# Performance work log

Hardware: AMD Instinct MI355X
Metric: run time of the kernel (lower is better)

Reference implementation:

```python
import jax, jax.numpy as jnp
import numpy as np

# ---- config (mirrors init_kwargs) ----
H = 128
W = 128
FMO_STEPS = 4
INPUT_FRAMES = 1
N_PIECES = 1
N_TERMS = 2
CAM_DIST = 2.0
ROT_DIVIDE = 1.0
SIGMAINV = 7000.0
ERODE_K = 5
FOCAL = float(1.0 / np.tan(1.57 / 4.0))  # generate_perspective_projection(1.57/2), aspect=1


def quaternion_to_angle_axis(q):
    # q: [B,4] in (w,x,y,z) convention (torchgeometry)
    q1, q2, q3 = q[..., 1], q[..., 2], q[..., 3]
    sin_sq = q1 * q1 + q2 * q2 + q3 * q3
    sin_t = jnp.sqrt(sin_sq + 1e-20)
    cos_t = q[..., 0]
    two_theta = 2.0 * jnp.where(cos_t < 0.0, jnp.arctan2(-sin_t, -cos_t), jnp.arctan2(sin_t, cos_t))
    k = jnp.where(sin_sq > 1e-12, two_theta / sin_t, 2.0)
    return q[..., 1:4] * k[..., None]


def angle_axis_to_rotation_matrix(aa):
    # aa: [B,3] -> [B,3,3] (Rodrigues)
    th = jnp.sqrt(jnp.sum(aa * aa, axis=-1, keepdims=True) + 1e-12)  # [B,1]
    k = aa / th
    kx, ky, kz = k[..., 0], k[..., 1], k[..., 2]
    zero = jnp.zeros_like(kx)
    K = jnp.stack([jnp.stack([zero, -kz, ky], -1),
                   jnp.stack([kz, zero, -kx], -1),
                   jnp.stack([-ky, kx, zero], -1)], -2)
    s = jnp.sin(th)[..., None]
    c = jnp.cos(th)[..., None]
    return jnp.eye(3, dtype=aa.dtype) + s * K + (1.0 - c) * jnp.matmul(K, K)


def rasterize(fv_img, fv_z, face_feat, fn_z):
    # fv_img [B,F,3,2] NDC, fv_z [B,F,3] camera z, face_feat [B,F,3,C], fn_z [B,F]
    B, F = fv_img.shape[:2]
    xs = jnp.linspace(-1.0, 1.0, W)
    ys = jnp.linspace(1.0, -1.0, H)
    py, px = jnp.meshgrid(ys, xs, indexing='ij')  # [H,W]
    a, b, c = fv_img[:, :, 0], fv_img[:, :, 1], fv_img[:, :, 2]  # [B,F,2]
    e0 = b - a
    e1 = c - a
    denom = e0[..., 0] * e1[..., 1] - e0[..., 1] * e1[..., 0]  # [B,F]
    valid = (fn_z > 0.0) & (jnp.abs(denom) > 1e-10)
    inv_den = jnp.where(jnp.abs(denom) > 1e-10, 1.0 / denom, 0.0)
    dx = px[None, None] - a[..., 0][..., None, None]  # [B,F,H,W]
    dy = py[None, None] - a[..., 1][..., None, None]
    w1 = (dx * e1[..., 1][..., None, None] - dy * e1[..., 0][..., None, None]) * inv_den[..., None, None]
    w2 = (e0[..., 0][..., None, None] * dy - e0[..., 1][..., None, None] * dx) * inv_den[..., None, None]
    w0 = 1.0 - w1 - w2
    inside = (w0 >= 0.0) & (w1 >= 0.0) & (w2 >= 0.0) & valid[..., None, None]
    zi = (w0 * fv_z[:, :, 0, None, None] + w1 * fv_z[:, :, 1, None, None] + w2 * fv_z[:, :, 2, None, None])
    score = jnp.where(inside, zi, -1e10)  # camera looks down -z: nearest face has max z
    best = jnp.argmax(score, axis=1)      # [B,H,W] z-buffer winner
    hit = jnp.any(inside, axis=1)
    bary = jnp.stack([w0, w1, w2], axis=-1)  # [B,F,H,W,3]
    idx = jnp.broadcast_to(best[:, None, :, :, None], (B, 1, H, W, 3))
    bary_b = jnp.take_along_axis(bary, idx, axis=1)[:, 0]  # [B,H,W,3]
    feat_b = jax.vmap(lambda f, i: f[i])(face_feat, best)  # [B,H,W,3,C]
    feats = jnp.einsum('bhwkc,bhwk->bhwc', feat_b, bary_b) * hit[..., None]
    # DIB-R soft silhouette: A = 1 - prod(1 - exp(-sigmainv*d^2)), d = dist to triangle, 0 inside
    d2 = None
    tri = (a, b, c)
    for i in range(3):
        p, q = tri[i], tri[(i + 1) % 3]
        ex = (q - p)[..., 0][..., None, None]
        ey = (q - p)[..., 1][..., None, None]
        rx = px[None, None] - p[..., 0][..., None, None]
        ry = py[None, None] - p[..., 1][..., None, None]
        L2 = ex * ex + ey * ey + 1e-12
        t = jnp.clip((rx * ex + ry * ey) / L2, 0.0, 1.0)
        dxe = rx - t * ex
        dye = ry - t * ey
        dd = dxe * dxe + dye * dye
        d2 = dd if d2 is None else jnp.minimum(d2, dd)
    d2 = jnp.where(inside, 0.0, d2)
    prob = jnp.where(valid[..., None, None], jnp.exp(-SIGMAINV * d2), 0.0)
    mask = 1.0 - jnp.prod(1.0 - prob, axis=1)  # [B,H,W]
    return feats, mask


def texture_sample(tex, uv):
    # tex [B,3,Th,Tw], uv [B,H,W,2] in [0,1]; bilinear, v axis flipped (image row 0 <-> v=1)
    Th, Tw = tex.shape[2], tex.shape[3]
    u = jnp.clip(uv[..., 0], 0.0, 1.0) * (Tw - 1)
    v = (1.0 - jnp.clip(uv[..., 1], 0.0, 1.0)) * (Th - 1)
    x0 = jnp.floor(u)
    y0 = jnp.floor(v)
    fx = (u - x0)[:, None]  # [B,1,H,W]
    fy = (v - y0)[:, None]
    x0i = jnp.clip(x0.astype(jnp.int32), 0, Tw - 1)
    x1i = jnp.clip(x0i + 1, 0, Tw - 1)
    y0i = jnp.clip(y0.astype(jnp.int32), 0, Th - 1)
    y1i = jnp.clip(y0i + 1, 0, Th - 1)
    g = jax.vmap(lambda t, yy, xx: t[:, yy, xx])  # [B,3,H,W]
    t00 = g(tex, y0i, x0i)
    t01 = g(tex, y0i, x1i)
    t10 = g(tex, y1i, x0i)
    t11 = g(tex, y1i, x1i)
    return t00 * (1 - fx) * (1 - fy) + t01 * fx * (1 - fy) + t10 * (1 - fx) * fy + t11 * fx * fy


def erode(m, k):
    # kornia erosion with an all-ones kxk kernel == min-pool (geodesic border)
    return -jax.lax.reduce_window(-m, -jnp.inf, jax.lax.max, (1, k, k), (1, 1, 1), 'SAME')


def render_frame(verts_world, faces, face_features, texture_maps):
    # camera at (0,0,CAM_DIST) looking at origin with up=(0,1,0): R_cam == I
    v_cam = verts_world - jnp.array([0.0, 0.0, CAM_DIST], dtype=verts_world.dtype)
    fv_cam = v_cam[:, faces]  # [B,F,3,3]
    n = jnp.cross(fv_cam[:, :, 1] - fv_cam[:, :, 0], fv_cam[:, :, 2] - fv_cam[:, :, 0])
    n = n / (jnp.linalg.norm(n, axis=-1, keepdims=True) + 1e-10)
    fn_z = n[..., 2]
    z = fv_cam[..., 2]  # negative in front of camera
    img = FOCAL * fv_cam[..., :2] / (-z[..., None] + 1e-10)  # [B,F,3,2]
    uv, mask = rasterize(img, z, face_features, fn_z)
    rgb = texture_sample(texture_maps, uv)  # [B,3,H,W]
    mask_e = erode(mask, ERODE_K)
    return jnp.concatenate([rgb, mask_e[:, None]], axis=1)  # [B,4,H,W]


def reference(vertices, translation, quaternion, exp, face_features, texture_maps, faces):
    rot = angle_axis_to_rotation_matrix(quaternion_to_angle_axis(quaternion[:, 0, 0]))
    trans_start = translation[:, :, 0, 0]  # [B,1,3]
    all_renders = []
    renders = []
    frames = 0
    time_before = 0.0
    for pind in range(N_PIECES):
        angles = quaternion_to_angle_axis(quaternion[:, pind, 1]) / ROT_DIVIDE
        rot_step = angle_axis_to_rotation_matrix(exp * angles / FMO_STEPS)
        rot_noexp = angle_axis_to_rotation_matrix(angles * (1.0 - exp))
        n_steps = FMO_STEPS * INPUT_FRAMES // N_PIECES  # prop[pind] (forced for single piece)
        for ti in np.linspace(0.0, 1.0, n_steps):
            if frames == 0:
                time_before = ti
            time_exp = time_before + (ti - time_before) * exp  # [1]
            verts = jnp.einsum('bij,bvj->bvi', rot, vertices) + trans_start
            for p in range(1, N_TERMS):
                verts = verts + (time_exp ** p) * translation[:, :, pind, p]
            renders.append(render_frame(verts, faces, face_features, texture_maps))
            frames += 1
            if frames == FMO_STEPS:
                frames = 0
                all_renders.append(jnp.stack(renders, 1))
                renders = []
                rot = jnp.matmul(rot, rot_noexp)
            else:
                rot = jnp.matmul(rot, rot_step)
        for p in range(1, N_TERMS):
            trans_start = trans_start + translation[:, :, pind, p]
    return jnp.stack(all_renders, 1)  # [B, input_frames, fmo_steps, 4, H, W]


def setup_inputs() -> dict:
    key = jax.random.key(0)
    ks = jax.random.split(key, 7)
    B, V, F = 1, 162, 320
    vertices = jax.random.normal(ks[0], (B, V, 3), jnp.float32) * 0.3
    translation = jax.random.normal(ks[1], (B, 1, N_PIECES, N_TERMS, 3), jnp.float32) * 0.1
    quaternion = jax.random.normal(ks[2], (B, N_PIECES, 2, 4), jnp.float32)
    exp = jax.random.uniform(ks[3], (1,), jnp.float32)
    face_features = jax.random.uniform(ks[4], (B, F, 3, 2), jnp.float32)
    texture_maps = jax.random.uniform(ks[5], (B, 3, 256, 256), jnp.float32)
    faces = jax.random.randint(ks[6], (F, 3), 0, V)
    return {"vertices": vertices, "translation": translation, "quaternion": quaternion,
            "exp": exp, "face_features": face_features, "texture_maps": texture_maps,
            "faces": faces}
```

## Files before the change

kernel.cpp:

```cpp
#include <hip/hip_runtime.h>
#include <math.h>

#define N_FRAMES 4
#define N_FACES  320
#define N_VERTS  162
#define IMG_H    128
#define IMG_W    128
#define NWAVES   8
#define FPW      40
#define REC_SZ   20

#define SV_OFF   0
#define BB_OFF   1952
#define BB_LD    48
#define REC_OFF  8096
#define ARENA_SZ 33696



__device__ __forceinline__ void q_to_aa(const float* q, float* aa) {
    float q1 = q[1], q2 = q[2], q3 = q[3];
    float sin_sq = (q1 * q1 + q2 * q2) + q3 * q3;
    float sin_t = sqrtf(sin_sq + 1e-20f);
    float cos_t = q[0];
    float two_theta = (cos_t < 0.0f) ? (2.0f * atan2f(-sin_t, -cos_t))
                                     : (2.0f * atan2f(sin_t, cos_t));
    float k = (sin_sq > 1e-12f) ? (two_theta / sin_t) : 2.0f;
    aa[0] = q1 * k; aa[1] = q2 * k; aa[2] = q3 * k;
}

__device__ __forceinline__ void aa_to_R(const float* aa, float* R) {
    float th = sqrtf(((aa[0] * aa[0] + aa[1] * aa[1]) + aa[2] * aa[2]) + 1e-12f);
    float kx = aa[0] / th, ky = aa[1] / th, kz = aa[2] / th;
    float K[9] = { 0.0f, -kz,  ky,
                   kz,  0.0f, -kx,
                  -ky,   kx, 0.0f };
    float s = sinf(th), c = cosf(th);
    float KK[9];
    for (int i = 0; i < 3; ++i)
        for (int j = 0; j < 3; ++j)
            KK[i*3+j] = (K[i*3+0] * K[0*3+j] + K[i*3+1] * K[1*3+j]) + K[i*3+2] * K[2*3+j];
    float omc = 1.0f - c;
    for (int i = 0; i < 9; ++i) {
        float eye = (i == 0 || i == 4 || i == 8) ? 1.0f : 0.0f;
        R[i] = (eye + s * K[i]) + omc * KK[i];
    }
}

__device__ __forceinline__ void mat3mul(const float* A, const float* B, float* C) {
    for (int i = 0; i < 3; ++i)
        for (int j = 0; j < 3; ++j)
            C[i*3+j] = (A[i*3+0] * B[0*3+j] + A[i*3+1] * B[1*3+j]) + A[i*3+2] * B[2*3+j];
}


__global__ void __launch_bounds__(512)
render_kernel(const float* __restrict__ verts_in,
              const float* __restrict__ transl,
              const float* __restrict__ quat,
              const float* __restrict__ expv,
              const int*   __restrict__ faces,
              const float* __restrict__ ffeat,
              const float* __restrict__ tex,
              float* __restrict__ out,
              float* __restrict__ maskbuf)
{
    __shared__ __align__(16) char arena[ARENA_SZ];
    __shared__ float rotS[9];
    float* sv   = (float*)(arena + SV_OFF);
    float* bb   = (float*)(arena + BB_OFF);
    float* recs = (float*)(arena + REC_OFF);
    float* red  = (float*)arena;

    int frame = blockIdx.x & 3;
    int blk   = blockIdx.x >> 2;
    int tid   = threadIdx.x;
    int lane  = tid & 63;
    int wv    = __builtin_amdgcn_readfirstlane(tid >> 6);
    int tile_x = blk & 7, tile_y = blk >> 3;
    int j = tile_x * 16 + (lane & 15);
    int i = tile_y * 4 + (lane >> 4);

    float e = expv[0];

    if (tid == 0) {
        float aa0[3], aa1[3], Rl[9], S[9];
        q_to_aa(quat, aa0);
        aa_to_R(aa0, Rl);
        q_to_aa(quat + 4, aa1);
        float arg[3];
        for (int t = 0; t < 3; ++t) arg[t] = (e * aa1[t]) / 4.0f;
        aa_to_R(arg, S);
        for (int t = 0; t < frame; ++t) {
            float nxt[9];
            mat3mul(Rl, S, nxt);
            for (int q = 0; q < 9; ++q) Rl[q] = nxt[q];
        }
        for (int q = 0; q < 9; ++q) rotS[q] = Rl[q];
    }
    __syncthreads();

    if (tid < N_VERTS) {
        float te = (float)((double)frame / 3.0) * e;
        float vx = verts_in[tid*3+0], vy = verts_in[tid*3+1], vz = verts_in[tid*3+2];
        float dx_ = (rotS[0] * vx + rotS[1] * vy) + rotS[2] * vz;
        float dy_ = (rotS[3] * vx + rotS[4] * vy) + rotS[5] * vz;
        float dz_ = (rotS[6] * vx + rotS[7] * vy) + rotS[8] * vz;
        float x = (dx_ + transl[0]) + te * transl[3];
        float y = (dy_ + transl[1]) + te * transl[4];
        float z = (dz_ + transl[2]) + te * transl[5];
        z = z - 2.0f;
        sv[tid*3+0] = x; sv[tid*3+1] = y; sv[tid*3+2] = z;
    }
    __syncthreads();

    const float FOCAL = (float)(1.0 / tan(1.57 / 4.0));
    int cnt;
    {
        bool valid = false;
        float ax=0, ay=0, bx=0, by=0, cx=0, cy=0, e0x=0, e0y=0, e1x=0, e1y=0;
        float e12x=0, e12y=0, z0=0, z1=0, z2=0, den=0;
        int f = wv * FPW + lane;
        if (lane < FPW) {
            int i0 = faces[f*3+0], i1 = faces[f*3+1], i2 = faces[f*3+2];
            const float* A = &sv[i0*3];
            const float* B = &sv[i1*3];
            const float* C = &sv[i2*3];
            float ux = B[0] - A[0], uy = B[1] - A[1];
            float wx = C[0] - A[0], wy = C[1] - A[1];
            float nz = ux * wy - uy * wx;
            float da = -A[2] + 1e-10f, db = -B[2] + 1e-10f, dc = -C[2] + 1e-10f;
            ax = (FOCAL * A[0]) / da; ay = (FOCAL * A[1]) / da;
            bx = (FOCAL * B[0]) / db; by = (FOCAL * B[1]) / db;
            cx = (FOCAL * C[0]) / dc; cy = (FOCAL * C[1]) / dc;
            e0x = bx - ax; e0y = by - ay;
            e1x = cx - ax; e1y = cy - ay;
            e12x = cx - bx; e12y = cy - by;
            den = e0x * e1y - e0y * e1x;
            z0 = A[2]; z1 = B[2]; z2 = C[2];
            valid = (fabsf(den) > 1e-10f) && (nz > 0.0f);
        }
        unsigned long long m = __ballot(valid);
        cnt = __popcll(m);
        if (valid) {
            unsigned long long lmask = (lane == 63) ? 0x7fffffffffffffffull
                                                    : ((1ull << lane) - 1ull);
            int pos = __popcll(m & lmask);
            float invden = 1.0f / den;
            float L2_0 = (e0x * e0x + e0y * e0y) + 1e-12f;
            float L2_1 = (e12x * e12x + e12y * e12y) + 1e-12f;
            float L2_2 = (e1x * e1x + e1y * e1y) + 1e-12f;
            float4* r = (float4*)&recs[(wv * FPW + pos) * REC_SZ];
            r[0] = make_float4(ax, ay, e0x, e0y);
            r[1] = make_float4(e1x, e1y, invden, (float)f);
            r[2] = make_float4(z0, z1, z2, 1.0f / L2_0);
            r[3] = make_float4(bx, by, e12x, e12y);
            r[4] = make_float4(cx, cy, 1.0f / L2_1, 1.0f / L2_2);
            float* wbb = &bb[wv * 4 * BB_LD];
            wbb[0*BB_LD + pos] = fminf(fminf(ax, bx), cx);
            wbb[1*BB_LD + pos] = fminf(fminf(ay, by), cy);
            wbb[2*BB_LD + pos] = fmaxf(fmaxf(ax, bx), cx);
            wbb[3*BB_LD + pos] = fmaxf(fmaxf(ay, by), cy);
        }
    }

    float px = (float)(-1.0 + 2.0 * (double)j / 127.0);
    float py = (float)( 1.0 - 2.0 * (double)i / 127.0);
    float txmin = (float)(-1.0 + 2.0 * (double)(tile_x * 16) / 127.0);
    float txmax = (float)(-1.0 + 2.0 * (double)(tile_x * 16 + 15) / 127.0);
    float tymax = (float)( 1.0 - 2.0 * (double)(tile_y * 4) / 127.0);
    float tymin = (float)( 1.0 - 2.0 * (double)(tile_y * 4 + 3) / 127.0);

    unsigned long long fmask;
    {
        int l = (lane < FPW) ? lane : 0;
        const float* wbb = &bb[wv * 4 * BB_LD];
        float xmin = wbb[0*BB_LD + l], ymin = wbb[1*BB_LD + l];
        float xmax = wbb[2*BB_LD + l], ymax = wbb[3*BB_LD + l];
        float cdx = fmaxf(fmaxf(xmin - txmax, txmin - xmax), 0.0f);
        float cdy = fmaxf(fmaxf(ymin - tymax, tymin - ymax), 0.0f);
        bool near = ((cdx * cdx + cdy * cdy) <= 0.0026f) && (lane < cnt);
        fmask = __ballot(near);
    }

    float best = -1e10f;
    int bestf = 0;
    float bw0 = 0.0f, bw1 = 0.0f, bw2 = 0.0f;
    float P = 1.0f;
    bool pzero = false;

    while (fmask) {
        int fc = __ffsll((unsigned long long)fmask) - 1;
        fmask &= fmask - 1;
        const float* d = &recs[(wv * FPW + fc) * REC_SZ];

        float ax = d[0], ay = d[1], e0x = d[2], e0y = d[3];
        float e1x = d[4], e1y = d[5], invden = d[6], fidx = d[7];
        float z0 = d[8], z1 = d[9], z2 = d[10];

        float dx = px - ax, dy = py - ay;
        float w1 = (dx * e1y - dy * e1x) * invden;
        float w2 = (e0x * dy - e0y * dx) * invden;
        float w0 = (1.0f - w1) - w2;
        bool inside = (w0 >= 0.0f) & (w1 >= 0.0f) & (w2 >= 0.0f);
        float zi = (w0 * z0 + w1 * z1) + w2 * z2;
        float score = inside ? zi : -1e10f;
        if (score > best) {
            best = score; bestf = (int)fidx; bw0 = w0; bw1 = w1; bw2 = w2;
        }

        if (!pzero) {
            float invL2_0 = d[11];
            float bx = d[12], by = d[13], e12x = d[14], e12y = d[15];
            float cx = d[16], cy = d[17], invL2_1 = d[18], invL2_2 = d[19];
            float t0 = fminf(fmaxf((dx * e0x + dy * e0y) * invL2_0, 0.0f), 1.0f);
            float x0 = dx - t0 * e0x, y0 = dy - t0 * e0y;
            float dd = x0 * x0 + y0 * y0;
            float rx1 = px - bx, ry1 = py - by;
            float t1 = fminf(fmaxf((rx1 * e12x + ry1 * e12y) * invL2_1, 0.0f), 1.0f);
            float x1 = rx1 - t1 * e12x, y1 = ry1 - t1 * e12y;
            dd = fminf(dd, x1 * x1 + y1 * y1);
            float ex2 = -e1x, ey2 = -e1y;
            float rx2 = px - cx, ry2 = py - cy;
            float t2 = fminf(fmaxf((rx2 * ex2 + ry2 * ey2) * invL2_2, 0.0f), 1.0f);
            float x2 = rx2 - t2 * ex2, y2 = ry2 - t2 * ey2;
            dd = fminf(dd, x2 * x2 + y2 * y2);

            float d2 = inside ? 0.0f : dd;
            float prob = __expf(-7000.0f * d2);
            P *= (1.0f - prob);
            pzero = __all(P == 0.0f);
        }
    }

    __syncthreads();
    float* my = &red[tid * 6];
    my[0] = best; my[1] = __int_as_float(bestf);
    my[2] = bw0;  my[3] = bw1; my[4] = bw2; my[5] = P;
    __syncthreads();

    if (tid < 64) {
        float bbst = red[tid * 6 + 0];
        int   bf   = __float_as_int(red[tid * 6 + 1]);
        float r0 = red[tid * 6 + 2], r1 = red[tid * 6 + 3], r2 = red[tid * 6 + 4];
        float Pt = red[tid * 6 + 5];
        for (int w = 1; w < NWAVES; ++w) {
            const float* s = &red[(w * 64 + tid) * 6];
            float sc = s[0]; int ff = __float_as_int(s[1]);
            if ((sc > bbst) || ((sc == bbst) && (ff < bf))) {
                bbst = sc; bf = ff; r0 = s[2]; r1 = s[3]; r2 = s[4];
            }
            Pt *= s[5];
        }

        bool hit = bbst != -1e10f;
        float uv0 = 0.0f, uv1 = 0.0f;
        if (hit) {
            const float* fp = ffeat + bf * 6;
            uv0 = (fp[0] * r0 + fp[2] * r1) + fp[4] * r2;
            uv1 = (fp[1] * r0 + fp[3] * r1) + fp[5] * r2;
        }
        float u = fminf(fmaxf(uv0, 0.0f), 1.0f) * 255.0f;
        float v = (1.0f - fminf(fmaxf(uv1, 0.0f), 1.0f)) * 255.0f;
        float x0f = floorf(u), y0f = floorf(v);
        float fx = u - x0f, fy = v - y0f;
        int x0i = min(max((int)x0f, 0), 255);
        int x1i = min(x0i + 1, 255);
        int y0i = min(max((int)y0f, 0), 255);
        int y1i = min(y0i + 1, 255);

        for (int c = 0; c < 3; ++c) {
            const float* tc = tex + c * 65536;
            float t00 = tc[y0i * 256 + x0i];
            float t01 = tc[y0i * 256 + x1i];
            float t10 = tc[y1i * 256 + x0i];
            float t11 = tc[y1i * 256 + x1i];
            float val = (t00 * (1.0f - fx)) * (1.0f - fy);
            val = val + (t01 * fx) * (1.0f - fy);
            val = val + (t10 * (1.0f - fx)) * fy;
            val = val + (t11 * fx) * fy;
            out[((frame * 4 + c) * IMG_H + i) * IMG_W + j] = val;
        }
        maskbuf[(frame * IMG_H + i) * IMG_W + j] = 1.0f - Pt;
    }
}


__global__ void __launch_bounds__(256)
erode_kernel(const float* __restrict__ maskbuf, float* __restrict__ out)
{
    int frame = blockIdx.x & 3;
    int pix = (blockIdx.x >> 2) * 256 + threadIdx.x;
    int i = pix >> 7, j = pix & 127;
    float m = 1e30f;
    for (int di = -2; di <= 2; ++di) {
        int ii = i + di;
        if (ii < 0 || ii >= IMG_H) continue;
        for (int dj = -2; dj <= 2; ++dj) {
            int jj = j + dj;
            if (jj < 0 || jj >= IMG_W) continue;
            m = fminf(m, maskbuf[(frame * IMG_H + ii) * IMG_W + jj]);
        }
    }
    out[((frame * 4 + 3) * IMG_H + i) * IMG_W + j] = m;
}


extern "C" void kernel_launch(void* const* d_in, const int* in_sizes, int n_in,
                              void* d_out, int out_size, void* d_ws, size_t ws_size,
                              hipStream_t stream) {
    const float* vertices      = (const float*)d_in[0];
    const float* translation   = (const float*)d_in[1];
    const float* quaternion    = (const float*)d_in[2];
    const float* expv          = (const float*)d_in[3];
    const float* face_features = (const float*)d_in[4];
    const float* texture_maps  = (const float*)d_in[5];
    const int*   faces         = (const int*)d_in[6];
    float* out = (float*)d_out;

    float* maskbuf = (float*)d_ws;

    render_kernel<<<N_FRAMES * 256, 512, 0, stream>>>(vertices, translation,
                                                      quaternion, expv, faces,
                                                      face_features, texture_maps,
                                                      out, maskbuf);
    erode_kernel<<<N_FRAMES * 64, 256, 0, stream>>>(maskbuf, out);
}
```

Measured before the change: 84.81 us.

## Cull faces before compaction and balance surviving faces evenly across waves

Moves the tile-bounding-box culling test ahead of record compaction, so only faces near the tile get written. A block-wide prefix sum over per-wave counts builds one shared list. The list is then split evenly across the 8 waves instead of each wave handling its own 40-face slice, which removes load imbalance when visible faces cluster in a few waves. It adds an extra __syncthreads and a small shared count array, and it drops the separate bbox arrays from shared memory.

```diff
diff --git a/kernel.cpp b/kernel.cpp
--- a/kernel.cpp
+++ b/kernel.cpp
@@ -11,10 +11,8 @@
 #define REC_SZ   20
 
 #define SV_OFF   0
-#define BB_OFF   1952
-#define BB_LD    48
-#define REC_OFF  8096
-#define ARENA_SZ 33696
+#define REC_OFF  1952
+#define ARENA_SZ 27552
 
 
 
@@ -67,8 +65,8 @@
 {
     __shared__ __align__(16) char arena[ARENA_SZ];
     __shared__ float rotS[9];
+    __shared__ int   cntS[NWAVES];
     float* sv   = (float*)(arena + SV_OFF);
-    float* bb   = (float*)(arena + BB_OFF);
     float* recs = (float*)(arena + REC_OFF);
     float* red  = (float*)arena;
 
@@ -114,10 +112,17 @@
     }
     __syncthreads();
 
+    float px = (float)(-1.0 + 2.0 * (double)j / 127.0);
+    float py = (float)( 1.0 - 2.0 * (double)i / 127.0);
+    float txmin = (float)(-1.0 + 2.0 * (double)(tile_x * 16) / 127.0);
+    float txmax = (float)(-1.0 + 2.0 * (double)(tile_x * 16 + 15) / 127.0);
+    float tymax = (float)( 1.0 - 2.0 * (double)(tile_y * 4) / 127.0);
+    float tymin = (float)( 1.0 - 2.0 * (double)(tile_y * 4 + 3) / 127.0);
+
     const float FOCAL = (float)(1.0 / tan(1.57 / 4.0));
-    int cnt;
+    int R, start, count;
     {
-        bool valid = false;
+        bool keep = false;
         float ax=0, ay=0, bx=0, by=0, cx=0, cy=0, e0x=0, e0y=0, e1x=0, e1y=0;
         float e12x=0, e12y=0, z0=0, z1=0, z2=0, den=0;
         int f = wv * FPW + lane;
@@ -138,49 +143,44 @@
             e12x = cx - bx; e12y = cy - by;
             den = e0x * e1y - e0y * e1x;
             z0 = A[2]; z1 = B[2]; z2 = C[2];
-            valid = (fabsf(den) > 1e-10f) && (nz > 0.0f);
-        }
-        unsigned long long m = __ballot(valid);
-        cnt = __popcll(m);
-        if (valid) {
+            bool valid = (fabsf(den) > 1e-10f) && (nz > 0.0f);
+            float xmin = fminf(fminf(ax, bx), cx);
+            float ymin = fminf(fminf(ay, by), cy);
+            float xmax = fmaxf(fmaxf(ax, bx), cx);
+            float ymax = fmaxf(fmaxf(ay, by), cy);
+            float cdx = fmaxf(fmaxf(xmin - txmax, txmin - xmax), 0.0f);
+            float cdy = fmaxf(fmaxf(ymin - tymax, tymin - ymax), 0.0f);
+            keep = valid && ((cdx * cdx + cdy * cdy) <= 0.0026f);
+        }
+        unsigned long long m = __ballot(keep);
+        if (lane == 0) cntS[wv] = __popcll(m);
+        __syncthreads();
+        int pre = 0; R = 0;
+        #pragma unroll
+        for (int w = 0; w < NWAVES; ++w) {
+            int c = cntS[w];
+            R += c;
+            if (w < wv) pre += c;
+        }
+        if (keep) {
             unsigned long long lmask = (lane == 63) ? 0x7fffffffffffffffull
                                                     : ((1ull << lane) - 1ull);
-            int pos = __popcll(m & lmask);
+            int pos = pre + __popcll(m & lmask);
             float invden = 1.0f / den;
             float L2_0 = (e0x * e0x + e0y * e0y) + 1e-12f;
             float L2_1 = (e12x * e12x + e12y * e12y) + 1e-12f;
             float L2_2 = (e1x * e1x + e1y * e1y) + 1e-12f;
-            float4* r = (float4*)&recs[(wv * FPW + pos) * REC_SZ];
+            float4* r = (float4*)&recs[pos * REC_SZ];
             r[0] = make_float4(ax, ay, e0x, e0y);
             r[1] = make_float4(e1x, e1y, invden, (float)f);
             r[2] = make_float4(z0, z1, z2, 1.0f / L2_0);
             r[3] = make_float4(bx, by, e12x, e12y);
             r[4] = make_float4(cx, cy, 1.0f / L2_1, 1.0f / L2_2);
-            float* wbb = &bb[wv * 4 * BB_LD];
-            wbb[0*BB_LD + pos] = fminf(fminf(ax, bx), cx);
-            wbb[1*BB_LD + pos] = fminf(fminf(ay, by), cy);
-            wbb[2*BB_LD + pos] = fmaxf(fmaxf(ax, bx), cx);
-            wbb[3*BB_LD + pos] = fmaxf(fmaxf(ay, by), cy);
-        }
-    }
-
-    float px = (float)(-1.0 + 2.0 * (double)j / 127.0);
-    float py = (float)( 1.0 - 2.0 * (double)i / 127.0);
-    float txmin = (float)(-1.0 + 2.0 * (double)(tile_x * 16) / 127.0);
-    float txmax = (float)(-1.0 + 2.0 * (double)(tile_x * 16 + 15) / 127.0);
-    float tymax = (float)( 1.0 - 2.0 * (double)(tile_y * 4) / 127.0);
-    float tymin = (float)( 1.0 - 2.0 * (double)(tile_y * 4 + 3) / 127.0);
-
-    unsigned long long fmask;
-    {
-        int l = (lane < FPW) ? lane : 0;
-        const float* wbb = &bb[wv * 4 * BB_LD];
-        float xmin = wbb[0*BB_LD + l], ymin = wbb[1*BB_LD + l];
-        float xmax = wbb[2*BB_LD + l], ymax = wbb[3*BB_LD + l];
-        float cdx = fmaxf(fmaxf(xmin - txmax, txmin - xmax), 0.0f);
-        float cdy = fmaxf(fmaxf(ymin - tymax, tymin - ymax), 0.0f);
-        bool near = ((cdx * cdx + cdy * cdy) <= 0.0026f) && (lane < cnt);
-        fmask = __ballot(near);
+        }
+        __syncthreads();
+        int q = R >> 3, rem = R & 7;
+        start = wv * q + min(wv, rem);
+        count = q + ((wv < rem) ? 1 : 0);
     }
 
     float best = -1e10f;
@@ -189,10 +189,8 @@
     float P = 1.0f;
     bool pzero = false;
 
-    while (fmask) {
-        int fc = __ffsll((unsigned long long)fmask) - 1;
-        fmask &= fmask - 1;
-        const float* d = &recs[(wv * FPW + fc) * REC_SZ];
+    for (int n = 0; n < count; ++n) {
+        const float* d = &recs[(start + n) * REC_SZ];
 
         float ax = d[0], ay = d[1], e0x = d[2], e0y = d[3];
         float e1x = d[4], e1y = d[5], invden = d[6], fidx = d[7];
```

Measured after the change: 82.46 us. -2.8%, faster.
